# Kernel tuning notes

Hardware: AMD Instinct MI355X
Metric: run time of the kernel (lower is better)

Reference implementation:

```python
import jax, jax.numpy as jnp
import numpy as np

# GPT-2 small structural constants (hardcoded in the original module)
L, H, D, DH, F, V, P, S, NC = 12, 12, 768, 64, 3072, 50257, 1024, 128, 29

def _ln(x, g, b, eps=1e-5):
    m = x.mean(-1, keepdims=True)
    v = ((x - m) ** 2).mean(-1, keepdims=True)
    return (x - m) * jax.lax.rsqrt(v + eps) * g + b

def _split_w(W):  # [D, D] -> [H, D, DH]: torch _split_heads on the last (output) dim
    return jnp.transpose(W.reshape(D, H, DH), (1, 0, 2))

def _attn_heads(xln, Wqh, Wkh, Wvh, Woh, qb, kb, vb, mask):
    # xln: [H, S, D] per-head circuit inputs. Computes the weight-product attention
    # branch: (xln@Wq+bq)(xln@Wk+bk)^T scores (algebraically identical to the four
    # W_mhqk bias-expanded terms in the source), causal softmax, then
    # attn @ ((xln@Wv+bv) @ W_mho) which equals attn@Output_mhov + attn@bv_Wo.
    q = jnp.einsum('hse,hed->hsd', xln, Wqh) + qb[:, None, :]
    k = jnp.einsum('hse,hed->hsd', xln, Wkh) + kb[:, None, :]
    v = jnp.einsum('hse,hed->hsd', xln, Wvh) + vb[:, None, :]
    s = jnp.einsum('hsd,htd->hst', q, k) / (DH ** 0.5)
    s = jnp.where(mask, s, jnp.finfo(s.dtype).min)
    a = jax.nn.softmax(s, axis=-1)
    ctx = jnp.einsum('hst,htd->hsd', a, v)
    return jnp.einsum('hsd,hdf->hsf', ctx, Woh)  # [H, S, D]

def _check1(x, r, records):
    # check_representation: subtract refined-matrix-gated recorded circuit tensors
    # from layers 0..i-1 (rows >= i of records are still zero, so full contraction
    # equals contracting records[0:i+1]).
    return x - jnp.einsum('lc,lcsd->sd', r, records)

def _checkH(x, rh, records):  # batched over the 12 per-head checks
    return x[None] - jnp.einsum('hlc,lcsd->hsd', rh, records)

def _forward(input_ids, refined_matrix, wte, wpe, qkv_w, qkv_b, proj_w, proj_b,
             ln1_g, ln1_b, ln2_g, ln2_b, fc_w, fc_b, mproj_w, mproj_b, lnf_g, lnf_b):
    rm = refined_matrix.astype(wte.dtype)                 # [L*NC, L, NC]
    h = wte[input_ids[0]] + wpe[:S]                       # [S, D]
    records = jnp.zeros((L, NC, S, D), dtype=h.dtype)     # record_circuit_tensor_all
    mask = jnp.tril(jnp.ones((S, S), dtype=bool))
    gelu = lambda x: jax.nn.gelu(x, approximate=True)     # GPT-2 gelu_new
    for i in range(L):
        Wq, Wk, Wv = jnp.split(qkv_w[i], 3, axis=1)
        Wqh, Wkh, Wvh = _split_w(Wq), _split_w(Wk), _split_w(Wv)
        qb = qkv_b[i][:D].reshape(H, DH)
        kb = qkv_b[i][D:2 * D].reshape(H, DH)
        vb = qkv_b[i][2 * D:].reshape(H, DH)
        Woh = proj_w[i].reshape(H, DH, D)                 # W_mho per head
        base = i * NC
        if i > 0:
            c1 = _check1(h, rm[base], records)                       # check 0
            x2 = _checkH(h, rm[base + 1:base + 1 + H], records)      # checks 1..12
            x3 = _check1(h, rm[base + 13], records)                  # check 13
            x4 = _checkH(h, rm[base + 14:base + 14 + H], records)    # checks 14..25
        else:
            c1, x3 = h, h
            x2 = jnp.broadcast_to(h, (H, S, D))
            x4 = x2
        # circuit 2: per-head attention via weight products
        x2ln = _ln(x2, ln1_g[i], ln1_b[i])
        head2 = _attn_heads(x2ln, Wqh, Wkh, Wvh, Woh, qb, kb, vb, mask)
        c2 = head2.sum(0)
        residual = c1 + c2 + proj_b[i]                    # + W_obias
        # full MLP stream on the residual (with c_fc bias, no c_proj bias)
        stream = gelu(_ln(residual, ln2_g[i], ln2_b[i]) @ fc_w[i] + fc_b[i]) @ mproj_w[i]
        # circuit 3: bias-free MLP of the (double-LN'd) checked layer input
        x3ln = _ln(_ln(x3, ln1_g[i], ln1_b[i]), ln2_g[i], ln2_b[i])
        c3 = gelu(x3ln @ fc_w[i]) @ mproj_w[i]
        # circuit 4: per-head attention branch -> MLP composition
        x4ln = _ln(x4, ln1_g[i], ln1_b[i])
        head4 = _attn_heads(x4ln, Wqh, Wkh, Wvh, Woh, qb, kb, vb, mask)
        c4_heads = gelu(_ln(head4, ln2_g[i], ln2_b[i]) @ fc_w[i]) @ mproj_w[i]
        c5 = stream - c3 - c4_heads.sum(0)                # nonlinearity compensation
        c6 = jnp.broadcast_to(mproj_b[i], (S, D))
        ob = jnp.broadcast_to(proj_b[i], (S, D))
        rec = jnp.concatenate([c1[None], head2, c3[None], c4_heads,
                               c5[None], c6[None], ob[None]], axis=0)  # [29, S, D]
        records = records.at[i].set(rec)
        h = residual + stream + mproj_b[i]
    return _ln(h, lnf_g, lnf_b) @ wte.T                   # logits [S, V]

def setup_inputs():
    key = jax.random.key(0)
    ks = jax.random.split(key, 16)
    sd = 0.02
    n = lambda k, shp: (jax.random.normal(k, shp) * sd).astype(jnp.float32)
    return {
        'input_ids': jax.random.randint(ks[0], (1, S), 0, V),
        'label_ids': jax.random.randint(ks[1], (1, S), 0, V),
        'refined_matrix': jax.random.randint(ks[2], (L * NC, L, NC), 0, 2).astype(jnp.int32),
        'wte': n(ks[3], (V, D)),
        'wpe': n(ks[4], (P, D)),
        'qkv_w': n(ks[5], (L, D, 3 * D)),
        'qkv_b': n(ks[6], (L, 3 * D)),
        'proj_w': n(ks[7], (L, D, D)),
        'proj_b': n(ks[8], (L, D)),
        'ln1_g': jnp.ones((L, D), jnp.float32),
        'ln1_b': jnp.zeros((L, D), jnp.float32),
        'ln2_g': jnp.ones((L, D), jnp.float32),
        'ln2_b': jnp.zeros((L, D), jnp.float32),
        'fc_w': n(ks[9], (L, D, F)),
        'fc_b': n(ks[10], (L, F)),
        'mproj_w': n(ks[11], (L, F, D)),
        'mproj_b': n(ks[12], (L, D)),
        'lnf_g': jnp.ones((D,), jnp.float32),
        'lnf_b': jnp.zeros((D,), jnp.float32),
    }

def reference(input_ids, label_ids, refined_matrix, wte, wpe, qkv_w, qkv_b, proj_w, proj_b,
              ln1_g, ln1_b, ln2_g, ln2_b, fc_w, fc_b, mproj_w, mproj_b, lnf_g, lnf_b):
    return _forward(input_ids, refined_matrix, wte, wpe, qkv_w, qkv_b, proj_w, proj_b,
                    ln1_g, ln1_b, ln2_g, ln2_b, fc_w, fc_b, mproj_w, mproj_b, lnf_g, lnf_b)
```

## Files before the change

kernel.cpp:

```cpp
#include <hip/hip_runtime.h>

#define SS 128
#define DD 768
#define HH 12
#define DHD 64
#define FF 3072
#define VV 50257
#define NCC 29
#define LL 12
#define SD (SS*DD)
#define SF (SS*FF)
#define TMAX (LL*NCC)

typedef unsigned short u16;
typedef __attribute__((ext_vector_type(8))) short short8;
typedef __attribute__((ext_vector_type(4))) float f32x4;

__device__ inline u16 f2bf(float f) {
    union { float f; unsigned u; } x; x.f = f;
    unsigned r = x.u + 0x7fffu + ((x.u >> 16) & 1u);
    return (u16)(r >> 16);
}

__global__ void k_masku(const int* __restrict__ rm, unsigned* __restrict__ lmu) {
    int idx = blockIdx.x * 256 + threadIdx.x;
    if (idx >= LL * TMAX) return;
    int i = idx / TMAX, t = idx % TMAX;
    unsigned m = 0;
    for (int j = 0; j < 26; j++)
        m |= (unsigned)(rm[(size_t)(i * NCC + j) * TMAX + t] & 1) << j;
    lmu[idx] = m;
}

__global__ void k_embed(const int* __restrict__ ids, const float* __restrict__ wte,
                        const float* __restrict__ wpe, float* __restrict__ h) {
    int sd = blockIdx.x * 256 + threadIdx.x;
    if (sd >= SD) return;
    int s = sd / DD, d = sd % DD;
    h[sd] = wte[(size_t)ids[s] * DD + d] + wpe[sd];
}

__global__ void k_cvt(const float* __restrict__ in, u16* __restrict__ out, int n4) {
    int i = blockIdx.x * 256 + threadIdx.x;
    if (i >= n4) return;
    float4 v = *(const float4*)(in + (size_t)i * 4);
    u16* o = out + (size_t)i * 4;
    o[0] = f2bf(v.x); o[1] = f2bf(v.y); o[2] = f2bf(v.z); o[3] = f2bf(v.w);
}

__global__ void k_qkvb(const float* __restrict__ qkv_b, float* __restrict__ qkvbp) {
    int idx = blockIdx.x * 256 + threadIdx.x;
    if (idx >= LL * 3 * DD) return;
    int l = idx / (3 * DD), r = idx % (3 * DD);
    int p = r / DD, rem = r % DD, h = rem / DHD, j = rem % DHD;
    qkvbp[(size_t)l * 3 * DD + h * 192 + p * DHD + j] = qkv_b[idx];
}

__global__ __launch_bounds__(256) void k_wt(const float* __restrict__ W, u16* __restrict__ WT,
                                            int K, int N, int remap,
                                            long long sW, long long sWT) {
    __shared__ float T[64][65];
    const float* Wb = W + (size_t)blockIdx.z * sW;
    u16* WTb = WT + (size_t)blockIdx.z * sWT;
    int n0 = blockIdx.x * 64, k0 = blockIdx.y * 64;
    int c = threadIdx.x & 63, r0 = threadIdx.x >> 6;
#pragma unroll
    for (int i = 0; i < 16; i++) {
        int r = r0 + 4 * i;
        T[r][c] = Wb[(size_t)(k0 + r) * N + n0 + c];
    }
    __syncthreads();
    int ob = n0 >> 6;
    if (remap) { int p = ob / 12, h = ob % 12; ob = h * 3 + p; }
    size_t orow0 = (size_t)ob * 64;
#pragma unroll
    for (int i = 0; i < 16; i++) {
        int a = r0 + 4 * i;
        WTb[(orow0 + a) * K + k0 + c] = f2bf(T[c][a]);
    }
}

__global__ __launch_bounds__(256) void k_check(
    const float* __restrict__ records, const unsigned* __restrict__ lmu,
    const float* __restrict__ h, float* __restrict__ rec0, float* __restrict__ x24,
    float* __restrict__ x3, int layer) {
    __shared__ float red[4][26][128];
    int lane = threadIdx.x & 63, w = threadIdx.x >> 6;
    int sd0 = blockIdx.x * 128;
    int sd = sd0 + lane * 2;
    int T = layer * NCC;
    int Tq = (T + 3) >> 2;
    int tb = w * Tq, te = tb + Tq; if (te > T) te = T;
    float2 acc[26];
#pragma unroll
    for (int j = 0; j < 26; j++) { acc[j].x = 0.f; acc[j].y = 0.f; }
    const unsigned* lm = lmu + layer * TMAX;
    const float* rp = records + sd;
    int t = tb;
    for (; t + 8 <= te; t += 8) {
        float2 r[8];
        unsigned mv[8];
#pragma unroll
        for (int u = 0; u < 8; u++) r[u] = *(const float2*)(rp + (size_t)(t + u) * SD);
#pragma unroll
        for (int u = 0; u < 8; u++) mv[u] = lm[t + u];
#pragma unroll
        for (int u = 0; u < 8; u++) {
            unsigned m = __builtin_amdgcn_readfirstlane(mv[u]);
#pragma unroll
            for (int j = 0; j < 26; j++) {
                float mm = (m & (1u << j)) ? 1.0f : 0.0f;
                acc[j].x = fmaf(mm, r[u].x, acc[j].x);
                acc[j].y = fmaf(mm, r[u].y, acc[j].y);
            }
        }
    }
    for (; t < te; t++) {
        float2 r = *(const float2*)(rp + (size_t)t * SD);
        unsigned m = __builtin_amdgcn_readfirstlane(lm[t]);
#pragma unroll
        for (int j = 0; j < 26; j++) {
            float mm = (m & (1u << j)) ? 1.0f : 0.0f;
            acc[j].x = fmaf(mm, r.x, acc[j].x);
            acc[j].y = fmaf(mm, r.y, acc[j].y);
        }
    }
#pragma unroll
    for (int j = 0; j < 26; j++)
        *(float2*)&red[w][j][lane * 2] = acc[j];
    __syncthreads();
    for (int o = threadIdx.x; o < 26 * 128; o += 256) {
        int j = o >> 7, sdl = o & 127;
        float s = red[0][j][sdl] + red[1][j][sdl] + red[2][j][sdl] + red[3][j][sdl];
        float v = h[sd0 + sdl] - s;
        float* dst;
        if (j == 0) dst = rec0;
        else if (j <= 12) dst = x24 + (size_t)(j - 1) * SD;
        else if (j == 13) dst = x3;
        else dst = x24 + (size_t)(12 + j - 14) * SD;
        dst[sd0 + sdl] = v;
    }
}

__device__ inline void wave_ln(float (&vals)[12], int lane, const float* __restrict__ g,
                               const float* __restrict__ b) {
    float s = 0.f;
#pragma unroll
    for (int i = 0; i < 12; i++) s += vals[i];
#pragma unroll
    for (int m = 32; m >= 1; m >>= 1) s += __shfl_xor(s, m, 64);
    float mean = s * (1.f / DD);
    float vs = 0.f;
#pragma unroll
    for (int i = 0; i < 12; i++) { float d = vals[i] - mean; vs += d * d; }
#pragma unroll
    for (int m = 32; m >= 1; m >>= 1) vs += __shfl_xor(vs, m, 64);
    float rstd = rsqrtf(vs * (1.f / DD) + 1e-5f);
#pragma unroll
    for (int i = 0; i < 12; i++)
        vals[i] = (vals[i] - mean) * rstd * g[lane + 64 * i] + b[lane + 64 * i];
}

__global__ __launch_bounds__(256) void k_ln(const float* __restrict__ in, float* __restrict__ outf,
                                            u16* __restrict__ outb,
                                            const float* __restrict__ g, const float* __restrict__ b,
                                            int R) {
    int row = blockIdx.x * 4 + (threadIdx.x >> 6);
    if (row >= R) return;
    int lane = threadIdx.x & 63;
    const float* x = in + (size_t)row * DD;
    float vals[12];
#pragma unroll
    for (int i = 0; i < 12; i++) vals[i] = x[lane + 64 * i];
    wave_ln(vals, lane, g, b);
#pragma unroll
    for (int i = 0; i < 12; i++) {
        int d = lane + 64 * i;
        if (outf) outf[(size_t)row * DD + d] = vals[i];
        if (outb) outb[(size_t)row * DD + d] = f2bf(vals[i]);
    }
}

__global__ __launch_bounds__(256) void k_rln(const float* __restrict__ reci,
                                             const float* __restrict__ x3,
                                             const float* __restrict__ tmp4,
                                             const float* __restrict__ proj_b_i,
                                             float* __restrict__ resid,
                                             u16* __restrict__ mlpAb,
                                             const float* __restrict__ l1g, const float* __restrict__ l1b,
                                             const float* __restrict__ l2g, const float* __restrict__ l2b) {
    int rowid = blockIdx.x * 4 + (threadIdx.x >> 6);
    int z = rowid >> 7, s = rowid & 127;
    int lane = threadIdx.x & 63;
    float vals[12];
    if (z == 0) {
        const float* src = x3 + (size_t)s * DD;
#pragma unroll
        for (int i = 0; i < 12; i++) vals[i] = src[lane + 64 * i];
        wave_ln(vals, lane, l1g, l1b);
    } else if (z <= 12) {
        const float* src = tmp4 + (size_t)(z - 1) * SD + (size_t)s * DD;
#pragma unroll
        for (int i = 0; i < 12; i++) vals[i] = src[lane + 64 * i];
    } else {
        const float* base = reci + (size_t)s * DD;
#pragma unroll
        for (int i = 0; i < 12; i++) {
            int d = lane + 64 * i;
            float a = base[d];
#pragma unroll
            for (int j = 1; j <= 12; j++) a += base[(size_t)j * SD + d];
            a += proj_b_i[d];
            vals[i] = a;
            resid[(size_t)s * DD + d] = a;
        }
    }
    wave_ln(vals, lane, l2g, l2b);
    u16* o = mlpAb + (size_t)z * SD + (size_t)s * DD;
#pragma unroll
    for (int i = 0; i < 12; i++) o[lane + 64 * i] = f2bf(vals[i]);
}

__global__ __launch_bounds__(256) void k_mm(
    const u16* __restrict__ A, const u16* __restrict__ BT,
    const float* __restrict__ bias, void* __restrict__ Cv, void* __restrict__ Cv2,
    int N, int K, int lda, int ldbt, int ldc,
    long long sA, long long sBT, long long sC, long long sBias,
    int zMod, int zHi, int biasLo, int mode) {
    __shared__ u16 As[128][40];
    __shared__ u16 Bs[64][40];
    int z = blockIdx.z;
    int zb = z % zMod;
    const u16* Ab = A + (size_t)z * sA;
    const u16* Bb = BT + (size_t)zb * sBT;
    int n0 = blockIdx.x * 64;
    int nSplit = gridDim.y;
    int kLen = K / nSplit;
    int kOff = blockIdx.y * kLen;
    int kEnd = kOff + kLen;
    int tid = threadIdx.x;
    int lane = tid & 63, wid = tid >> 6;
    int wm = (wid >> 1) * 64, wn = (wid & 1) * 32;
    int l15 = lane & 15, l4 = lane >> 4;
    int sr = tid >> 2, sseg = tid & 3;
    int bn = n0 + sr;
    f32x4 acc[4][2];
#pragma unroll
    for (int i = 0; i < 4; i++) { acc[i][0] = (f32x4)0.f; acc[i][1] = (f32x4)0.f; }
    uint4 zero; zero.x = 0u; zero.y = 0u; zero.z = 0u; zero.w = 0u;
    uint4 a0 = *(const uint4*)(Ab + (size_t)sr * lda + kOff + sseg * 8);
    uint4 a1 = *(const uint4*)(Ab + (size_t)(sr + 64) * lda + kOff + sseg * 8);
    uint4 bv = (bn < N) ? *(const uint4*)(Bb + (size_t)bn * ldbt + kOff + sseg * 8) : zero;
    for (int k0 = kOff; k0 < kEnd; k0 += 32) {
        __syncthreads();
        *(uint4*)&As[sr][sseg * 8] = a0;
        *(uint4*)&As[sr + 64][sseg * 8] = a1;
        *(uint4*)&Bs[sr][sseg * 8] = bv;
        __syncthreads();
        if (k0 + 32 < kEnd) {
            a0 = *(const uint4*)(Ab + (size_t)sr * lda + k0 + 32 + sseg * 8);
            a1 = *(const uint4*)(Ab + (size_t)(sr + 64) * lda + k0 + 32 + sseg * 8);
            bv = (bn < N) ? *(const uint4*)(Bb + (size_t)bn * ldbt + k0 + 32 + sseg * 8) : zero;
        }
        short8 af[4], bfr[2];
#pragma unroll
        for (int i = 0; i < 4; i++) af[i] = *(const short8*)&As[wm + i * 16 + l15][l4 * 8];
#pragma unroll
        for (int j = 0; j < 2; j++) bfr[j] = *(const short8*)&Bs[wn + j * 16 + l15][l4 * 8];
#pragma unroll
        for (int i = 0; i < 4; i++)
#pragma unroll
            for (int j = 0; j < 2; j++)
                acc[i][j] = __builtin_amdgcn_mfma_f32_16x16x32_bf16(af[i], bfr[j], acc[i][j], 0, 0, 0);
    }
    const float* bp = (bias != nullptr && z >= biasLo) ? bias + (size_t)zb * sBias : nullptr;
    void* Cuse;
    int zc;
    if (nSplit > 1) { Cuse = Cv; zc = z * nSplit + blockIdx.y; }
    else { Cuse = (z >= zHi) ? Cv2 : Cv; zc = (z >= zHi) ? z - zHi : z; }
    if (mode == 0) {
        float* Cb = (float*)Cuse + (size_t)zc * sC;
#pragma unroll
        for (int i = 0; i < 4; i++) {
            int row = wm + i * 16 + l4 * 4;
#pragma unroll
            for (int j = 0; j < 2; j++) {
                int col = n0 + wn + j * 16 + l15;
                if (col >= N) continue;
                float bb = bp ? bp[col] : 0.f;
#pragma unroll
                for (int r = 0; r < 4; r++)
                    Cb[(size_t)(row + r) * ldc + col] = acc[i][j][r] + bb;
            }
        }
    } else {
        u16* Cb = (u16*)Cuse + (size_t)zc * sC;
#pragma unroll
        for (int i = 0; i < 4; i++) {
            int row = wm + i * 16 + l4 * 4;
#pragma unroll
            for (int j = 0; j < 2; j++) {
                int col = n0 + wn + j * 16 + l15;
                if (col >= N) continue;
                float bb = bp ? bp[col] : 0.f;
#pragma unroll
                for (int r = 0; r < 4; r++) {
                    float v = acc[i][j][r] + bb;
                    float c = v + 0.044715f * v * v * v;
                    float gv = 0.5f * v * (1.f + tanhf(0.7978845608028654f * c));
                    Cb[(size_t)(row + r) * ldc + col] = f2bf(gv);
                }
            }
        }
    }
}

__global__ __launch_bounds__(256) void k_attnp(const float* __restrict__ qkvp,
                                               const float* __restrict__ qbias,
                                               const u16* __restrict__ projT,
                                               float* __restrict__ outLo,
                                               float* __restrict__ outHi) {
    __shared__ float kv[SS * DHD];
    __shared__ float qs[16][DHD];
    __shared__ float sc[16][130];
    __shared__ u16 cxs[16][72];
    int z = blockIdx.y, s0 = blockIdx.x * 16;
    int hb = z % 12;
    const float* p0 = qkvp + (size_t)z * 4 * (SS * 192);
    const float* p1 = p0 + SS * 192;
    const float* p2 = p1 + SS * 192;
    const float* p3 = p2 + SS * 192;
    const float* qb = qbias + (size_t)hb * 192;
    int tid = threadIdx.x;
    for (int idx = tid; idx < SS * DHD; idx += 256) {
        int t = idx >> 6, d = idx & 63;
        int o = t * 192 + 64 + d;
        kv[idx] = p0[o] + p1[o] + p2[o] + p3[o] + qb[64 + d];
    }
    for (int idx = tid; idx < 16 * DHD; idx += 256) {
        int r = idx >> 6, d = idx & 63;
        int o = (s0 + r) * 192 + d;
        qs[r][d] = p0[o] + p1[o] + p2[o] + p3[o] + qb[d];
    }
    __syncthreads();
    int r = tid >> 4, tt = tid & 15;
    int s = s0 + r;
    float pl[8];
#pragma unroll
    for (int u = 0; u < 8; u++) {
        int t = tt + 16 * u;
        float dot;
        if (t <= s) {
            dot = 0.f;
            for (int d = 0; d < DHD; d++) dot += qs[r][d] * kv[t * DHD + d];
            dot *= 0.125f;
        } else {
            dot = -1e30f;
        }
        pl[u] = dot;
    }
    float mx = pl[0];
#pragma unroll
    for (int u = 1; u < 8; u++) mx = fmaxf(mx, pl[u]);
#pragma unroll
    for (int m = 1; m < 16; m <<= 1) mx = fmaxf(mx, __shfl_xor(mx, m, 16));
    float sum = 0.f;
#pragma unroll
    for (int u = 0; u < 8; u++) { pl[u] = __expf(pl[u] - mx); sum += pl[u]; }
#pragma unroll
    for (int m = 1; m < 16; m <<= 1) sum += __shfl_xor(sum, m, 16);
    float inv = 1.f / sum;
#pragma unroll
    for (int u = 0; u < 8; u++) sc[r][tt + 16 * u] = pl[u] * inv;
    __syncthreads();
    for (int idx = tid; idx < SS * DHD; idx += 256) {
        int t = idx >> 6, d = idx & 63;
        int o = t * 192 + 128 + d;
        kv[idx] = p0[o] + p1[o] + p2[o] + p3[o] + qb[128 + d];
    }
    __syncthreads();
    int d = tid & 63, r0 = tid >> 6;
#pragma unroll
    for (int u = 0; u < 4; u++) {
        int rr = r0 + 4 * u;
        float a = 0.f;
        for (int t = 0; t < SS; t++) a += sc[rr][t] * kv[t * DHD + d];
        cxs[rr][d] = f2bf(a);
    }
    __syncthreads();
    int lane = tid & 63, w = tid >> 6;
    int l15 = lane & 15, l4 = lane >> 4;
    short8 af[2];
#pragma unroll
    for (int ks = 0; ks < 2; ks++) af[ks] = *(const short8*)&cxs[l15][ks * 32 + l4 * 8];
    float* ob = (z < 12) ? outLo + (size_t)z * SD : outHi + (size_t)(z - 12) * SD;
#pragma unroll
    for (int nt = 0; nt < 12; nt++) {
        int n0t = (w * 12 + nt) * 16;
        f32x4 acc = (f32x4)0.f;
#pragma unroll
        for (int ks = 0; ks < 2; ks++) {
            short8 bf = *(const short8*)(projT + (size_t)(n0t + l15) * DD + hb * DHD + ks * 32 + l4 * 8);
            acc = __builtin_amdgcn_mfma_f32_16x16x32_bf16(af[ks], bf, acc, 0, 0, 0);
        }
#pragma unroll
        for (int rr = 0; rr < 4; rr++)
            ob[(size_t)(s0 + l4 * 4 + rr) * DD + n0t + l15] = acc[rr];
    }
}

__global__ void k_red(const float* __restrict__ part, const float* __restrict__ resid,
                      const float* __restrict__ proj_b_i, const float* __restrict__ mproj_b_i,
                      float* __restrict__ reci, float* __restrict__ h) {
    int sd = blockIdx.x * 256 + threadIdx.x;
    if (sd >= SD) return;
    int d = sd % DD;
    float v0 = 0.f, s4 = 0.f, st = 0.f;
#pragma unroll
    for (int zz = 0; zz < 14; zz++) {
        const float* p = part + (size_t)zz * 4 * SD + sd;
        float v = p[0] + p[SD] + p[2 * SD] + p[3 * SD];
        if (zz == 0) { v0 = v; reci[(size_t)13 * SD + sd] = v; }
        else if (zz <= 12) { s4 += v; reci[(size_t)(13 + zz) * SD + sd] = v; }
        else st = v;
    }
    reci[(size_t)26 * SD + sd] = st - v0 - s4;
    reci[(size_t)27 * SD + sd] = mproj_b_i[d];
    reci[(size_t)28 * SD + sd] = proj_b_i[d];
    h[sd] = resid[sd] + st + mproj_b_i[d];
}

extern "C" void kernel_launch(void* const* d_in, const int* in_sizes, int n_in,
                              void* d_out, int out_size, void* d_ws, size_t ws_size,
                              hipStream_t stream) {
    const int* ids = (const int*)d_in[0];
    const int* rm = (const int*)d_in[2];
    const float* wte = (const float*)d_in[3];
    const float* wpe = (const float*)d_in[4];
    const float* qkv_w = (const float*)d_in[5];
    const float* qkv_b = (const float*)d_in[6];
    const float* proj_w = (const float*)d_in[7];
    const float* proj_b = (const float*)d_in[8];
    const float* ln1_g = (const float*)d_in[9];
    const float* ln1_b = (const float*)d_in[10];
    const float* ln2_g = (const float*)d_in[11];
    const float* ln2_b = (const float*)d_in[12];
    const float* fc_w = (const float*)d_in[13];
    const float* fc_b = (const float*)d_in[14];
    const float* mproj_w = (const float*)d_in[15];
    const float* mproj_b = (const float*)d_in[16];
    const float* lnf_g = (const float*)d_in[17];
    const float* lnf_b = (const float*)d_in[18];
    float* out = (float*)d_out;

    float* ws = (float*)d_ws;
    size_t off = 0;
    float* records = ws + off; off += (size_t)LL * NCC * SD;
    float* x24  = ws + off; off += (size_t)24 * SD;
    float* tmp4 = ws + off; off += (size_t)12 * SD;
    float* h    = ws + off; off += SD;
    float* x3   = ws + off; off += SD;
    float* resid= ws + off; off += SD;
    float* qkvp = ws + off; off += (size_t)24 * 4 * SS * 192;
    float* mpp  = ws + off; off += (size_t)14 * 4 * SD;
    float* qkvbp= ws + off; off += (size_t)LL * 3 * DD;
    u16* xlnb  = (u16*)(ws + off); off += (size_t)24 * SD / 2;
    u16* mlpAb = (u16*)(ws + off); off += (size_t)14 * SD / 2;
    u16* hfcb  = (u16*)(ws + off); off += (size_t)14 * SF / 2;
    u16* lnfb  = (u16*)(ws + off); off += SD / 2;
    u16* qkvhT = (u16*)(ws + off); off += (size_t)LL * 2304 * DD / 2;
    u16* fcT   = (u16*)(ws + off); off += (size_t)LL * FF * DD / 2;
    u16* mprojT= (u16*)(ws + off); off += (size_t)LL * DD * FF / 2;
    u16* projT = (u16*)(ws + off); off += (size_t)LL * DD * DD / 2;
    u16* wteb  = (u16*)(ws + off); off += (size_t)VV * DD / 2;
    unsigned* lmu = (unsigned*)(ws + off);

    k_masku<<<(LL * TMAX + 255) / 256, 256, 0, stream>>>(rm, lmu);
    k_embed<<<SD / 256, 256, 0, stream>>>(ids, wte, wpe, h);
    k_cvt<<<((VV * DD / 4) + 255) / 256, 256, 0, stream>>>(wte, wteb, VV * DD / 4);
    k_qkvb<<<(LL * 3 * DD + 255) / 256, 256, 0, stream>>>(qkv_b, qkvbp);
    k_wt<<<dim3(36, 12, 12), 256, 0, stream>>>(qkv_w, qkvhT, DD, 3 * DD, 1,
                                               (long long)DD * 3 * DD, (long long)2304 * DD);
    k_wt<<<dim3(48, 12, 12), 256, 0, stream>>>(fc_w, fcT, DD, FF, 0,
                                               (long long)DD * FF, (long long)FF * DD);
    k_wt<<<dim3(12, 48, 12), 256, 0, stream>>>(mproj_w, mprojT, FF, DD, 0,
                                               (long long)FF * DD, (long long)DD * FF);
    k_wt<<<dim3(12, 12, 12), 256, 0, stream>>>(proj_w, projT, DD, DD, 0,
                                               (long long)DD * DD, (long long)DD * DD);

    for (int i = 0; i < LL; i++) {
        float* reci = records + (size_t)i * NCC * SD;
        const float* l1g = ln1_g + i * DD; const float* l1b = ln1_b + i * DD;
        const float* l2g = ln2_g + i * DD; const float* l2b = ln2_b + i * DD;
        const u16* qkvhTi = qkvhT + (size_t)i * 2304 * DD;
        const u16* fcTi = fcT + (size_t)i * FF * DD;
        const u16* mprojTi = mprojT + (size_t)i * DD * FF;
        const u16* projTi = projT + (size_t)i * DD * DD;

        k_check<<<SD / 128, 256, 0, stream>>>(records, lmu, h, reci, x24, x3, i);

        k_ln<<<24 * SS / 4, 256, 0, stream>>>(x24, nullptr, xlnb, l1g, l1b, 24 * SS);
        k_mm<<<dim3(3, 4, 24), 256, 0, stream>>>(
            xlnb, qkvhTi, nullptr, qkvp, nullptr,
            192, DD, DD, DD, 192, SD, (long long)192 * DD, (long long)SS * 192, 0, 12, 9999, 99, 0);
        k_attnp<<<dim3(SS / 16, 24), 256, 0, stream>>>(qkvp, qkvbp + (size_t)i * 3 * DD,
                                                       projTi, reci + SD, tmp4);
        k_rln<<<14 * SS / 4, 256, 0, stream>>>(reci, x3, tmp4, proj_b + i * DD, resid, mlpAb,
                                               l1g, l1b, l2g, l2b);
        k_mm<<<dim3(48, 1, 14), 256, 0, stream>>>(
            mlpAb, fcTi, fc_b + (size_t)i * FF, hfcb, nullptr,
            FF, DD, DD, DD, FF, SD, 0, SF, 0, 1, 9999, 13, 1);
        k_mm<<<dim3(12, 4, 14), 256, 0, stream>>>(
            hfcb, mprojTi, nullptr, mpp, nullptr,
            DD, FF, FF, FF, DD, SF, 0, SD, 0, 1, 9999, 99, 0);
        k_red<<<SD / 256, 256, 0, stream>>>(mpp, resid, proj_b + i * DD, mproj_b + i * DD,
                                            reci, h);
    }

    k_ln<<<SS / 4, 256, 0, stream>>>(h, nullptr, lnfb, lnf_g, lnf_b, SS);
    k_mm<<<dim3((VV + 63) / 64, 1, 1), 256, 0, stream>>>(
        lnfb, wteb, nullptr, out, nullptr,
        VV, DD, DD, DD, VV, 0, 0, 0, 0, 1, 9999, 99, 0);
}
```

Measured before the change: 1.803 ms.

## Fold bias record slots into precomputed per-layer bias corrections in check

Record slots 27 and 28 only hold broadcast bias vectors, so they are no longer stored. A one-time kernel precomputes, for each layer and each check index, the refined-mask-weighted sum of earlier mproj and proj biases over D. k_check then contracts 27 slots per layer instead of 29 and subtracts the small precomputed bias term. This cuts the records traffic in the check contraction, which grows with layer count, and drops two full SD writes per layer in k_red. In exchange it adds a setup kernel and splits the LDS reduction into two passes to halve shared memory.

Measured after the change: 1.820 ms. No clear change (+1.0%).

```diff
diff --git a/kernel.cpp b/kernel.cpp
--- a/kernel.cpp
+++ b/kernel.cpp
@@ -7,10 +7,12 @@
 #define FF 3072
 #define VV 50257
 #define NCC 29
+#define NCR 27
 #define LL 12
 #define SD (SS*DD)
 #define SF (SS*FF)
 #define TMAX (LL*NCC)
+#define TRMAX (LL*NCR)
 
 typedef unsigned short u16;
 typedef __attribute__((ext_vector_type(8))) short short8;
@@ -24,12 +26,29 @@
 
 __global__ void k_masku(const int* __restrict__ rm, unsigned* __restrict__ lmu) {
     int idx = blockIdx.x * 256 + threadIdx.x;
-    if (idx >= LL * TMAX) return;
-    int i = idx / TMAX, t = idx % TMAX;
+    if (idx >= LL * TRMAX) return;
+    int i = idx / TRMAX, t = idx % TRMAX;
+    int l = t / NCR, c = t % NCR;
     unsigned m = 0;
     for (int j = 0; j < 26; j++)
-        m |= (unsigned)(rm[(size_t)(i * NCC + j) * TMAX + t] & 1) << j;
+        m |= (unsigned)(rm[(size_t)(i * NCC + j) * TMAX + l * NCC + c] & 1) << j;
     lmu[idx] = m;
+}
+
+__global__ void k_bias(const int* __restrict__ rm, const float* __restrict__ proj_b,
+                       const float* __restrict__ mproj_b, float* __restrict__ bc) {
+    int idx = blockIdx.x * 256 + threadIdx.x;
+    if (idx >= LL * 26 * DD) return;
+    int i = idx / (26 * DD);
+    int r = idx % (26 * DD);
+    int j = r / DD, d = r % DD;
+    float s = 0.f;
+    for (int l = 0; l < i; l++) {
+        const int* row = rm + (size_t)(i * NCC + j) * TMAX + l * NCC;
+        s += (float)(row[27] & 1) * mproj_b[(size_t)l * DD + d];
+        s += (float)(row[28] & 1) * proj_b[(size_t)l * DD + d];
+    }
+    bc[idx] = s;
 }
 
 __global__ void k_embed(const int* __restrict__ ids, const float* __restrict__ wte,
@@ -82,19 +101,21 @@
 
 __global__ __launch_bounds__(256) void k_check(
     const float* __restrict__ records, const unsigned* __restrict__ lmu,
+    const float* __restrict__ bc,
     const float* __restrict__ h, float* __restrict__ rec0, float* __restrict__ x24,
     float* __restrict__ x3, int layer) {
-    __shared__ float red[4][26][128];
+    __shared__ float red[4][13][128];
     int lane = threadIdx.x & 63, w = threadIdx.x >> 6;
     int sd0 = blockIdx.x * 128;
+    int d0 = sd0 % DD;
     int sd = sd0 + lane * 2;
-    int T = layer * NCC;
+    int T = layer * NCR;
     int Tq = (T + 3) >> 2;
     int tb = w * Tq, te = tb + Tq; if (te > T) te = T;
     float2 acc[26];
 #pragma unroll
     for (int j = 0; j < 26; j++) { acc[j].x = 0.f; acc[j].y = 0.f; }
-    const unsigned* lm = lmu + layer * TMAX;
+    const unsigned* lm = lmu + layer * TRMAX;
     const float* rp = records + sd;
     int t = tb;
     for (; t + 8 <= te; t += 8) {
@@ -125,20 +146,27 @@
             acc[j].y = fmaf(mm, r.y, acc[j].y);
         }
     }
-#pragma unroll
-    for (int j = 0; j < 26; j++)
-        *(float2*)&red[w][j][lane * 2] = acc[j];
-    __syncthreads();
-    for (int o = threadIdx.x; o < 26 * 128; o += 256) {
-        int j = o >> 7, sdl = o & 127;
-        float s = red[0][j][sdl] + red[1][j][sdl] + red[2][j][sdl] + red[3][j][sdl];
-        float v = h[sd0 + sdl] - s;
-        float* dst;
-        if (j == 0) dst = rec0;
-        else if (j <= 12) dst = x24 + (size_t)(j - 1) * SD;
-        else if (j == 13) dst = x3;
-        else dst = x24 + (size_t)(12 + j - 14) * SD;
-        dst[sd0 + sdl] = v;
+    const float* bcl = bc + (size_t)layer * 26 * DD;
+#pragma unroll
+    for (int pass = 0; pass < 2; pass++) {
+        int jb = pass * 13;
+#pragma unroll
+        for (int j2 = 0; j2 < 13; j2++)
+            *(float2*)&red[w][j2][lane * 2] = acc[jb + j2];
+        __syncthreads();
+        for (int o = threadIdx.x; o < 13 * 128; o += 256) {
+            int j2 = o >> 7, sdl = o & 127;
+            int j = jb + j2;
+            float s = red[0][j2][sdl] + red[1][j2][sdl] + red[2][j2][sdl] + red[3][j2][sdl];
+            float v = h[sd0 + sdl] - s - bcl[(size_t)j * DD + d0 + sdl];
+            float* dst;
+            if (j == 0) dst = rec0;
+            else if (j <= 12) dst = x24 + (size_t)(j - 1) * SD;
+            else if (j == 13) dst = x3;
+            else dst = x24 + (size_t)(12 + j - 14) * SD;
+            dst[sd0 + sdl] = v;
+        }
+        __syncthreads();
     }
 }
 
@@ -410,7 +438,7 @@
 }
 
 __global__ void k_red(const float* __restrict__ part, const float* __restrict__ resid,
-                      const float* __restrict__ proj_b_i, const float* __restrict__ mproj_b_i,
+                      const float* __restrict__ mproj_b_i,
                       float* __restrict__ reci, float* __restrict__ h) {
     int sd = blockIdx.x * 256 + threadIdx.x;
     if (sd >= SD) return;
@@ -425,8 +453,6 @@
         else st = v;
     }
     reci[(size_t)26 * SD + sd] = st - v0 - s4;
-    reci[(size_t)27 * SD + sd] = mproj_b_i[d];
-    reci[(size_t)28 * SD + sd] = proj_b_i[d];
     h[sd] = resid[sd] + st + mproj_b_i[d];
 }
 
@@ -455,7 +481,7 @@
 
     float* ws = (float*)d_ws;
     size_t off = 0;
-    float* records = ws + off; off += (size_t)LL * NCC * SD;
+    float* records = ws + off; off += (size_t)LL * NCR * SD;
     float* x24  = ws + off; off += (size_t)24 * SD;
     float* tmp4 = ws + off; off += (size_t)12 * SD;
     float* h    = ws + off; off += SD;
@@ -464,6 +490,7 @@
     float* qkvp = ws + off; off += (size_t)24 * 4 * SS * 192;
     float* mpp  = ws + off; off += (size_t)14 * 4 * SD;
     float* qkvbp= ws + off; off += (size_t)LL * 3 * DD;
+    float* bc   = ws + off; off += (size_t)LL * 26 * DD;
     u16* xlnb  = (u16*)(ws + off); off += (size_t)24 * SD / 2;
     u16* mlpAb = (u16*)(ws + off); off += (size_t)14 * SD / 2;
     u16* hfcb  = (u16*)(ws + off); off += (size_t)14 * SF / 2;
@@ -475,7 +502,8 @@
     u16* wteb  = (u16*)(ws + off); off += (size_t)VV * DD / 2;
     unsigned* lmu = (unsigned*)(ws + off);
 
-    k_masku<<<(LL * TMAX + 255) / 256, 256, 0, stream>>>(rm, lmu);
+    k_masku<<<(LL * TRMAX + 255) / 256, 256, 0, stream>>>(rm, lmu);
+    k_bias<<<(LL * 26 * DD + 255) / 256, 256, 0, stream>>>(rm, proj_b, mproj_b, bc);
     k_embed<<<SD / 256, 256, 0, stream>>>(ids, wte, wpe, h);
     k_cvt<<<((VV * DD / 4) + 255) / 256, 256, 0, stream>>>(wte, wteb, VV * DD / 4);
     k_qkvb<<<(LL * 3 * DD + 255) / 256, 256, 0, stream>>>(qkv_b, qkvbp);
@@ -489,7 +517,7 @@
                                                (long long)DD * DD, (long long)DD * DD);
 
     for (int i = 0; i < LL; i++) {
-        float* reci = records + (size_t)i * NCC * SD;
+        float* reci = records + (size_t)i * NCR * SD;
         const float* l1g = ln1_g + i * DD; const float* l1b = ln1_b + i * DD;
         const float* l2g = ln2_g + i * DD; const float* l2b = ln2_b + i * DD;
         const u16* qkvhTi = qkvhT + (size_t)i * 2304 * DD;
@@ -497,7 +525,7 @@
         const u16* mprojTi = mprojT + (size_t)i * DD * FF;
         const u16* projTi = projT + (size_t)i * DD * DD;
 
-        k_check<<<SD / 128, 256, 0, stream>>>(records, lmu, h, reci, x24, x3, i);
+        k_check<<<SD / 128, 256, 0, stream>>>(records, lmu, bc, h, reci, x24, x3, i);
 
         k_ln<<<24 * SS / 4, 256, 0, stream>>>(x24, nullptr, xlnb, l1g, l1b, 24 * SS);
         k_mm<<<dim3(3, 4, 24), 256, 0, stream>>>(
@@ -513,8 +541,7 @@
         k_mm<<<dim3(12, 4, 14), 256, 0, stream>>>(
             hfcb, mprojTi, nullptr, mpp, nullptr,
             DD, FF, FF, FF, DD, SF, 0, SD, 0, 1, 9999, 99, 0);
-        k_red<<<SD / 256, 256, 0, stream>>>(mpp, resid, proj_b + i * DD, mproj_b + i * DD,
-                                            reci, h);
+        k_red<<<SD / 256, 256, 0, stream>>>(mpp, resid, mproj_b + i * DD, reci, h);
     }
 
     k_ln<<<SS / 4, 256, 0, stream>>>(h, nullptr, lnfb, lnf_g, lnf_b, SS);
```
